# Kernel optimization log

Hardware: AMD Instinct MI355X
Metric: run time of the kernel (lower is better)

## Reference

```python
import jax, jax.numpy as jnp
import numpy as np

N_ITER = 50  # default n_iter in entmax_bisect


def _entmax_bisect(X, alpha):
    """alpha-entmax via bisection (Peters et al.), over last axis.
    X: [..., d]; alpha: broadcastable to X[..., :1], values in (1, 2].
    """
    am1 = alpha - 1.0
    inv = 1.0 / am1
    Xs = X * am1
    d = X.shape[-1]
    max_val = jnp.max(Xs, axis=-1, keepdims=True)
    tau_lo = max_val - 1.0                      # max - gp(1, alpha)
    tau_hi = max_val - (1.0 / d) ** am1          # max - gp(1/d, alpha)  [note: gp(x)=x**(1/am1); (1/d)**(1/(1/am1))? see below]
    # gp(x, alpha) = x ** (1 / (alpha - 1)); so gp(1/d) = (1/d) ** inv
    tau_hi = max_val - (1.0 / d) ** inv
    f_lo = jnp.sum(jnp.clip(Xs - tau_lo, 0.0, None) ** inv, axis=-1, keepdims=True) - 1.0
    dm0 = tau_hi - tau_lo

    def step(carry, _):
        tau_lo, dm, _tau_m = carry
        dm = dm * 0.5
        tau_m = tau_lo + dm
        p_m = jnp.clip(Xs - tau_m, 0.0, None) ** inv
        f_m = jnp.sum(p_m, axis=-1, keepdims=True) - 1.0
        tau_lo = jnp.where(f_m * f_lo >= 0.0, tau_m, tau_lo)
        return (tau_lo, dm, tau_m), None

    (tau_lo, dm, tau_m), _ = jax.lax.scan(step, (tau_lo, dm0, tau_lo), None, length=N_ITER)
    p = jnp.clip(Xs - tau_m, 0.0, None) ** inv
    # ensure_sum_one=True
    return p / jnp.sum(p, axis=-1, keepdims=True)


def setup_inputs() -> dict:
    key = jax.random.key(0)
    k1, k2 = jax.random.split(key)
    B, H, Q, K = 4, 16, 1024, 1024
    att_scores = jax.random.normal(k1, (B, H, Q, K), dtype=jnp.float32)
    alpha = jax.random.uniform(k2, (H,), dtype=jnp.float32)  # raw in (0,1); mapped to (1.01, 1.99) inside reference
    return {"att_scores": att_scores, "alpha": alpha}


def reference(att_scores, alpha):
    # torch module: per-head alpha in [1.01, 2] (clamp(1+sigmoid(pre_alpha))).
    a = (1.01 + 0.98 * alpha).reshape(1, -1, 1, 1)  # [1, H, 1, 1], broadcasts over B, Q, K
    return _entmax_bisect(att_scores, a)
```

## Files before the change

### kernel.cpp

```cpp
#include <hip/hip_runtime.h>


typedef float f4 __attribute__((ext_vector_type(4)));

template <int CTRL, int RM>
__device__ __forceinline__ float dpp_add(float x) {
  int s = __builtin_amdgcn_update_dpp(0, __builtin_bit_cast(int, x),
                                      CTRL, RM, 0xF, false);
  return x + __builtin_bit_cast(float, s);
}
template <int CTRL, int RM>
__device__ __forceinline__ float dpp_max(float x) {
  int s = __builtin_amdgcn_update_dpp((int)0xFF800000,
                                      __builtin_bit_cast(int, x),
                                      CTRL, RM, 0xF, false);
  return fmaxf(x, __builtin_bit_cast(float, s));
}
__device__ __forceinline__ float wave_sum(float x) {
  x = dpp_add<0xB1, 0xF>(x);
  x = dpp_add<0x4E, 0xF>(x);
  x = dpp_add<0x141, 0xF>(x);
  x = dpp_add<0x140, 0xF>(x);
  x = dpp_add<0x142, 0xA>(x);
  x = dpp_add<0x143, 0xC>(x);
  return __builtin_bit_cast(float,
      __builtin_amdgcn_readlane(__builtin_bit_cast(int, x), 63));
}
__device__ __forceinline__ float wave_max(float x) {
  x = dpp_max<0xB1, 0xF>(x);
  x = dpp_max<0x4E, 0xF>(x);
  x = dpp_max<0x141, 0xF>(x);
  x = dpp_max<0x140, 0xF>(x);
  x = dpp_max<0x142, 0xA>(x);
  x = dpp_max<0x143, 0xC>(x);
  return __builtin_bit_cast(float,
      __builtin_amdgcn_readlane(__builtin_bit_cast(int, x), 63));
}

#define MAXIT 12

__global__ __launch_bounds__(256) void entmax_iqi(
    const float* __restrict__ X, const float* __restrict__ A,
    float* __restrict__ O, int nrows) {
  __shared__ float          cval[4][1024];
  __shared__ unsigned short cidx[4][1024];

  const int lane = threadIdx.x & 63;
  const int wid  = threadIdx.x >> 6;
  const long long row = (long long)blockIdx.x * 4 + wid;
  if (row >= nrows) return;

  const f4* xr4 = reinterpret_cast<const f4*>(X + row * 1024);
  f4* or4       = reinterpret_cast<f4*>(O + row * 1024);

  const int h = (int)((row >> 10) & 15);
  const float a   = 1.01f + 0.98f * A[h];
  const float am1 = a - 1.0f;
  const float inv = 1.0f / am1;
  const float c1  = inv - 1.0f;

  float xs[16];
#pragma unroll
  for (int c = 0; c < 4; ++c) {
    f4 t = __builtin_nontemporal_load(xr4 + c * 64 + lane);
    xs[4*c+0] = t.x * am1; xs[4*c+1] = t.y * am1;
    xs[4*c+2] = t.z * am1; xs[4*c+3] = t.w * am1;
  }
  float m = xs[0];
#pragma unroll
  for (int j = 1; j < 16; ++j) m = fmaxf(m, xs[j]);
  m = wave_max(m);
#pragma unroll
  for (int j = 0; j < 16; ++j) xs[j] -= m;

  int nact = 0;
#pragma unroll
  for (int j = 0; j < 16; ++j)
    nact += (int)__popcll(__ballot(xs[j] > -1.0f));
  const int  K      = (nact + 63) >> 6;
  const bool direct = (K == 16);

  float vals[16];
  if (direct) {
#pragma unroll
    for (int k = 0; k < 16; ++k) vals[k] = xs[k];
  } else {
    int base = 0;
#pragma unroll
    for (int c = 0; c < 4; ++c) {
#pragma unroll
      for (int k = 0; k < 4; ++k) {
        const int j = 4*c + k;
        const bool act = xs[j] > -1.0f;
        const unsigned long long mk = __ballot(act);
        if (act) {
          const int pos = base + __popcll(mk & ((1ull << lane) - 1ull));
          cval[wid][pos] = xs[j];
          cidx[wid][pos] = (unsigned short)(c * 256 + lane * 4 + k);
        }
        base += __popcll(mk);
      }
    }
    for (int pos = nact + lane; pos < (K << 6); pos += 64)
      cval[wid][pos] = -2.0f;
    asm volatile("s_waitcnt lgkmcnt(0)" ::: "memory");
#pragma unroll
    for (int k = 0; k < 16; ++k)
      if (k < K) vals[k] = cval[wid][lane + (k << 6)];
  }

  float lwlo = -10.0f * am1;
  float lwhi = 0.0f;
  float w = 1.0f, lw = 0.0f;
  float p[16];
  float f, lw_p, lf_p;
  float lw_pp = 0.0f, lf_pp = 0.0f;
  bool have2 = false;
  {
    float fs = 0.0f, gs = 0.0f;
#pragma unroll
    for (int k = 0; k < 16; ++k)
      if (k < K) {
        float u  = fmaxf(vals[k] + 1.0f, 0.0f);
        float e  = __builtin_amdgcn_exp2f(c1 * __builtin_amdgcn_logf(u));
        float pe = e * u;
        p[k] = pe; fs += pe; gs += e;
      }
    f = wave_sum(fs);
    const float g = wave_sum(gs);
    lw_p = 0.0f; lf_p = __builtin_amdgcn_logf(f);
    if (fabsf(f - 1.0f) > 1e-6f) {
      float lwn = -lf_p * f * am1 / g;
      if (!(lwn > lwlo) || !(lwn < lwhi)) lwn = 0.5f * (lwlo + lwhi);
      w = __builtin_amdgcn_exp2f(lwn); lw = lwn;

      for (int it = 1; it < MAXIT; ++it) {
        float fs2 = 0.0f;
#pragma unroll
        for (int k = 0; k < 16; ++k)
          if (k < K) {
            float u  = fmaxf(vals[k] + w, 0.0f);
            float pe = __builtin_amdgcn_exp2f(
                inv * __builtin_amdgcn_logf(u));
            p[k] = pe; fs2 += pe;
          }
        f = wave_sum(fs2);

        float lwnew;
        if (f > 0.0f) {
          if (fabsf(f - 1.0f) <= 1e-6f) break;
          const float lf = __builtin_amdgcn_logf(f);
          if (f > 1.0f) lwhi = lw; else lwlo = lw;

          float cand = 0.0f; bool got = false;
          if (have2) {
            const float d01 = lf - lf_p, d02 = lf - lf_pp, d12 = lf_p - lf_pp;
            const float r01 = __builtin_amdgcn_rcpf(d01);
            const float r02 = __builtin_amdgcn_rcpf(d02);
            const float r12 = __builtin_amdgcn_rcpf(d12);
            cand = lw    * lf_p * lf_pp * r01 * r02
                 - lw_p  * lf   * lf_pp * r01 * r12
                 + lw_pp * lf   * lf_p  * r02 * r12;
            got = (cand > lwlo) && (cand < lwhi);
          }
          if (!got) {
            const float si = (lw - lw_p) / (lf - lf_p);
            cand = lw - lf * si;
            if (!(si > 0.0f) || !(cand > lwlo) || !(cand < lwhi))
              cand = 0.5f * (lwlo + lwhi);
          }
          lw_pp = lw_p; lf_pp = lf_p; lw_p = lw; lf_p = lf; have2 = true;
          lwnew = cand;
        } else {
          lwlo = lw;
          lwnew = 0.5f * (lwlo + lwhi);
        }
        const float wnew  = __builtin_amdgcn_exp2f(lwnew);
        if (!(fabsf(wnew - w) > 2e-5f * fmaxf(fabsf(m - w), 1.0f))) break;
        w = wnew; lw = lwnew;
      }
    }
  }

  const float r = 1.0f / f;
  if (direct) {
#pragma unroll
    for (int c = 0; c < 4; ++c) {
      f4 t;
      t.x = p[4*c+0] * r; t.y = p[4*c+1] * r;
      t.z = p[4*c+2] * r; t.w = p[4*c+3] * r;
      __builtin_nontemporal_store(t, or4 + c * 64 + lane);
    }
  } else {
    const f4 z = {0.0f, 0.0f, 0.0f, 0.0f};
#pragma unroll
    for (int c = 0; c < 4; ++c)
      reinterpret_cast<f4*>(&cval[wid][0])[c * 64 + lane] = z;
    asm volatile("s_waitcnt lgkmcnt(0)" ::: "memory");
#pragma unroll
    for (int k = 0; k < 16; ++k)
      if (k < K) {
        const int pos = lane + (k << 6);
        if (pos < nact) cval[wid][cidx[wid][pos]] = p[k] * r;
      }
    asm volatile("s_waitcnt lgkmcnt(0)" ::: "memory");
#pragma unroll
    for (int c = 0; c < 4; ++c) {
      f4 t = reinterpret_cast<const f4*>(&cval[wid][0])[c * 64 + lane];
      __builtin_nontemporal_store(t, or4 + c * 64 + lane);
    }
  }
}

extern "C" void kernel_launch(void* const* d_in, const int* in_sizes, int n_in,
                              void* d_out, int out_size, void* d_ws, size_t ws_size,
                              hipStream_t stream) {
  const float* X = (const float*)d_in[0];
  const float* A = (const float*)d_in[1];
  float* O       = (float*)d_out;
  const int nrows = in_sizes[0] / 1024;
  const int blocks = (nrows + 3) / 4;
  hipLaunchKernelGGL(entmax_iqi, dim3(blocks), dim3(256), 0, stream,
                     X, A, O, nrows);
}
```

Baseline: 93.93 us.

## Drop index scratch array and raise occupancy via launch bounds and register reuse

Removes the per-wave ushort index array in LDS and rebuilds the scatter by replaying the ballot-based compaction from a per-lane active bitmask, so the output is gathered with writes in order instead of scattered. It also reuses the xs registers for the compacted values rather than a separate vals array, and adds a min-blocks hint of 8 to launch_bounds. Together these cut LDS and register footprint to allow more resident waves for this memory-bound kernel. The tradeoff is 16 extra ballots in the output phase and possible register spilling under the tighter bound.

After: 97.27 us. 1.04x slower.

```diff
diff --git a/kernel.cpp b/kernel.cpp
--- a/kernel.cpp
+++ b/kernel.cpp
@@ -39,11 +39,10 @@
 
 #define MAXIT 12
 
-__global__ __launch_bounds__(256) void entmax_iqi(
+__global__ __launch_bounds__(256, 8) void entmax_occ(
     const float* __restrict__ X, const float* __restrict__ A,
     float* __restrict__ O, int nrows) {
-  __shared__ float          cval[4][1024];
-  __shared__ unsigned short cidx[4][1024];
+  __shared__ float cval[4][1024];
 
   const int lane = threadIdx.x & 63;
   const int wid  = threadIdx.x >> 6;
@@ -63,8 +62,8 @@
 #pragma unroll
   for (int c = 0; c < 4; ++c) {
     f4 t = __builtin_nontemporal_load(xr4 + c * 64 + lane);
-    xs[4*c+0] = t.x * am1; xs[4*c+1] = t.y * am1;
-    xs[4*c+2] = t.z * am1; xs[4*c+3] = t.w * am1;
+    xs[4*c+0] = t[0] * am1; xs[4*c+1] = t[1] * am1;
+    xs[4*c+2] = t[2] * am1; xs[4*c+3] = t[3] * am1;
   }
   float m = xs[0];
 #pragma unroll
@@ -73,40 +72,32 @@
 #pragma unroll
   for (int j = 0; j < 16; ++j) xs[j] -= m;
 
-  int nact = 0;
-#pragma unroll
-  for (int j = 0; j < 16; ++j)
-    nact += (int)__popcll(__ballot(xs[j] > -1.0f));
+  int actmask = 0, nact = 0;
+#pragma unroll
+  for (int j = 0; j < 16; ++j) {
+    const bool act = xs[j] > -1.0f;
+    if (act) actmask |= (1 << j);
+    nact += (int)__popcll(__ballot(act));
+  }
   const int  K      = (nact + 63) >> 6;
   const bool direct = (K == 16);
 
-  float vals[16];
-  if (direct) {
-#pragma unroll
-    for (int k = 0; k < 16; ++k) vals[k] = xs[k];
-  } else {
+  if (!direct) {
     int base = 0;
 #pragma unroll
-    for (int c = 0; c < 4; ++c) {
-#pragma unroll
-      for (int k = 0; k < 4; ++k) {
-        const int j = 4*c + k;
-        const bool act = xs[j] > -1.0f;
-        const unsigned long long mk = __ballot(act);
-        if (act) {
-          const int pos = base + __popcll(mk & ((1ull << lane) - 1ull));
-          cval[wid][pos] = xs[j];
-          cidx[wid][pos] = (unsigned short)(c * 256 + lane * 4 + k);
-        }
-        base += __popcll(mk);
-      }
+    for (int j = 0; j < 16; ++j) {
+      const bool act = (actmask >> j) & 1;
+      const unsigned long long mk = __ballot(act);
+      if (act)
+        cval[wid][base + __popcll(mk & ((1ull << lane) - 1ull))] = xs[j];
+      base += __popcll(mk);
     }
     for (int pos = nact + lane; pos < (K << 6); pos += 64)
       cval[wid][pos] = -2.0f;
     asm volatile("s_waitcnt lgkmcnt(0)" ::: "memory");
 #pragma unroll
     for (int k = 0; k < 16; ++k)
-      if (k < K) vals[k] = cval[wid][lane + (k << 6)];
+      if (k < K) xs[k] = cval[wid][lane + (k << 6)];
   }
 
   float lwlo = -10.0f * am1;
@@ -121,7 +112,7 @@
 #pragma unroll
     for (int k = 0; k < 16; ++k)
       if (k < K) {
-        float u  = fmaxf(vals[k] + 1.0f, 0.0f);
+        float u  = fmaxf(xs[k] + 1.0f, 0.0f);
         float e  = __builtin_amdgcn_exp2f(c1 * __builtin_amdgcn_logf(u));
         float pe = e * u;
         p[k] = pe; fs += pe; gs += e;
@@ -139,7 +130,7 @@
 #pragma unroll
         for (int k = 0; k < 16; ++k)
           if (k < K) {
-            float u  = fmaxf(vals[k] + w, 0.0f);
+            float u  = fmaxf(xs[k] + w, 0.0f);
             float pe = __builtin_amdgcn_exp2f(
                 inv * __builtin_amdgcn_logf(u));
             p[k] = pe; fs2 += pe;
@@ -187,26 +178,31 @@
 #pragma unroll
     for (int c = 0; c < 4; ++c) {
       f4 t;
-      t.x = p[4*c+0] * r; t.y = p[4*c+1] * r;
-      t.z = p[4*c+2] * r; t.w = p[4*c+3] * r;
+      t[0] = p[4*c+0] * r; t[1] = p[4*c+1] * r;
+      t[2] = p[4*c+2] * r; t[3] = p[4*c+3] * r;
       __builtin_nontemporal_store(t, or4 + c * 64 + lane);
     }
   } else {
-    const f4 z = {0.0f, 0.0f, 0.0f, 0.0f};
-#pragma unroll
-    for (int c = 0; c < 4; ++c)
-      reinterpret_cast<f4*>(&cval[wid][0])[c * 64 + lane] = z;
+#pragma unroll
+    for (int k = 0; k < 16; ++k)
+      if (k < K) cval[wid][lane + (k << 6)] = p[k] * r;
     asm volatile("s_waitcnt lgkmcnt(0)" ::: "memory");
-#pragma unroll
-    for (int k = 0; k < 16; ++k)
-      if (k < K) {
-        const int pos = lane + (k << 6);
-        if (pos < nact) cval[wid][cidx[wid][pos]] = p[k] * r;
+    int base = 0;
+#pragma unroll
+    for (int c = 0; c < 4; ++c) {
+      float tmp[4];
+#pragma unroll
+      for (int k = 0; k < 4; ++k) {
+        const int j = 4*c + k;
+        const bool act = (actmask >> j) & 1;
+        const unsigned long long mk = __ballot(act);
+        float v = 0.0f;
+        if (act) v = cval[wid][base + __popcll(mk & ((1ull << lane) - 1ull))];
+        base += __popcll(mk);
+        tmp[k] = v;
       }
-    asm volatile("s_waitcnt lgkmcnt(0)" ::: "memory");
-#pragma unroll
-    for (int c = 0; c < 4; ++c) {
-      f4 t = reinterpret_cast<const f4*>(&cval[wid][0])[c * 64 + lane];
+      f4 t;
+      t[0] = tmp[0]; t[1] = tmp[1]; t[2] = tmp[2]; t[3] = tmp[3];
       __builtin_nontemporal_store(t, or4 + c * 64 + lane);
     }
   }
@@ -220,6 +216,6 @@
   float* O       = (float*)d_out;
   const int nrows = in_sizes[0] / 1024;
   const int blocks = (nrows + 3) / 4;
-  hipLaunchKernelGGL(entmax_iqi, dim3(blocks), dim3(256), 0, stream,
+  hipLaunchKernelGGL(entmax_occ, dim3(blocks), dim3(256), 0, stream,
                      X, A, O, nrows);
 }
```
